# Optimization experiments

Hardware: AMD Instinct MI355X
Metric: run time of the kernel (lower is better)

## Reference

```python
import jax, jax.numpy as jnp
import numpy as np

L = 4
B_LIST = [30, 17, 9, 5, 3]      # bandwidth schedule (geometric 30 -> 3)
F_LIST = [1, 2, 5, 12, 28, 64]  # channel schedule (geometric 1 -> 64)
BATCH = 32
C64 = jnp.complex64

# near-identity grids (beta = pi/16, 6 alphas; SO3 grid additionally 6 gammas)
_A6 = np.linspace(0.0, 2 * np.pi, 6, endpoint=False)
S2_BETA = np.full(6, np.pi / 16)
S2_ALPHA = _A6
_aa, _gg = np.meshgrid(_A6, _A6, indexing='ij')
SO3_ALPHA = _aa.ravel()
SO3_BETA = np.full(36, np.pi / 16)
SO3_GAMMA = _gg.ravel()


def betas_of(b):
    return np.pi * (2 * np.arange(2 * b) + 1) / (4 * b)


def quad_weights(b):
    j = np.arange(2 * b)
    k = np.arange(b)
    s = (np.sin(np.pi * np.outer(2 * j + 1, 2 * k + 1) / (4 * b)) / (2 * k + 1)).sum(1)
    return (2.0 / b) * np.sin(np.pi * (2 * j + 1) / (4 * b)) * s


def wigner_d_all(lmax, betas):
    """Wigner small-d d^l_{m',m}(beta) via exp(-i beta Jy); list_l of [nbeta,2l+1,2l+1]."""
    out = [np.ones((len(betas), 1, 1))]
    for l in range(1, lmax):
        m = np.arange(-l, l)
        jp = np.sqrt(l * (l + 1) - m * (m + 1))  # <m+1|J+|m>
        Jy = np.zeros((2 * l + 1, 2 * l + 1), np.complex128)
        i = np.arange(2 * l)
        Jy[i + 1, i] = -0.5j * jp
        Jy[i, i + 1] = 0.5j * jp
        lam, U = np.linalg.eigh(Jy)
        ph = np.exp(-1j * np.outer(betas, lam))
        out.append(np.einsum('ak,bk,ck->bac', U, ph, U.conj()).real)
    return out


def fft_idx(l, n):
    # indices of frequencies m = -l..l in fft ordering of length n
    return np.concatenate([np.arange(n - l, n), np.arange(l + 1)])


def s2_fft(x, b_out):
    # x: [B,f,2b,2b] real (beta,alpha) -> list_l of [B,f,2l+1] complex
    b_in = x.shape[-1] // 2
    wig = wigner_d_all(b_out, betas_of(b_in))
    w = quad_weights(b_in)
    xf = jnp.fft.fft(x, axis=-1)
    out = []
    for l in range(b_out):
        dl = jnp.asarray((wig[l][:, :, l] * w[:, None]).astype(np.complex64))  # [2b,2l+1]
        out.append(jnp.einsum('bfjm,jm->bfm', xf[..., fft_idx(l, 2 * b_in)], dl))
    return out


def so3_fft(x, b_out):
    # x: [B,f,2b,2b,2b] real (beta,alpha,gamma) -> list_l of [B,f,2l+1,2l+1]
    b_in = x.shape[-1] // 2
    wig = wigner_d_all(b_out, betas_of(b_in))
    w = quad_weights(b_in)
    xf = jnp.fft.fft2(x, axes=(-2, -1))
    out = []
    for l in range(b_out):
        idx = fft_idx(l, 2 * b_in)
        dl = jnp.asarray((wig[l] * w[:, None, None]).astype(np.complex64))
        out.append(jnp.einsum('bfjmn,jmn->bfmn', xf[:, :, :, idx[:, None], idx[None, :]], dl))
    return out


def so3_ifft(coeffs, b):
    # coeffs: list_l [B,f,2l+1,2l+1] -> real signal [B,f,2b,2b,2b]
    wig = wigner_d_all(b, betas_of(b))
    nb = 2 * b
    Bz, f = coeffs[0].shape[:2]
    X = jnp.zeros((Bz, f, nb, nb, nb), C64)
    for l in range(b):
        idx = fft_idx(l, nb)
        dl = jnp.asarray(((2 * l + 1) * wig[l]).astype(np.complex64))
        X = X.at[:, :, :, idx[:, None], idx[None, :]].add(
            jnp.einsum('bfmn,jmn->bfjmn', coeffs[l], dl))
    return (jnp.fft.ifft2(X, axes=(-2, -1)) * (nb * nb)).real


def s2_kernel_ft(k, b):
    # k: [f_in,f_out,P] -> list_l of [2l+1,f_in,f_out] complex
    wig = wigner_d_all(b, S2_BETA)
    kc = k.astype(C64)
    out = []
    for l in range(b):
        m = np.arange(-l, l + 1)
        F = (wig[l][:, :, l] * np.exp(1j * np.outer(S2_ALPHA, m))).astype(np.complex64)
        out.append(jnp.einsum('iop,pm->mio', kc, jnp.asarray(F)))
    return out


def so3_kernel_ft(k, b):
    # k: [f_in,f_out,P] -> list_l of [2l+1,2l+1,f_in,f_out] complex
    wig = wigner_d_all(b, SO3_BETA)
    kc = k.astype(C64)
    out = []
    for l in range(b):
        m = np.arange(-l, l + 1)
        F = (wig[l]
             * np.exp(1j * np.outer(SO3_ALPHA, m))[:, :, None]
             * np.exp(1j * np.outer(SO3_GAMMA, m))[:, None, :]).astype(np.complex64)
        out.append(jnp.einsum('iop,pmn->mnio', kc, jnp.asarray(F)))
    return out


def s2_conv(x, kern, b_out):
    xh = s2_fft(x, b_out)
    kh = s2_kernel_ft(kern, b_out)
    yh = [jnp.einsum('bim,nio->bomn', xh[l], kh[l].conj()) for l in range(b_out)]
    return so3_ifft(yh, b_out)


def so3_conv(x, kern, b_out):
    xh = so3_fft(x, b_out)
    kh = so3_kernel_ft(kern, b_out)
    yh = [jnp.einsum('bimk,nkio->bomn', xh[l], kh[l].conj()) for l in range(b_out)]
    return so3_ifft(yh, b_out)


def so3_integrate(x):
    b = x.shape[-1] // 2
    w = jnp.asarray(quad_weights(b).astype(np.float32))
    return jnp.einsum('bfjac,j->bf', x, w) / float((2 * b) ** 2)


def batchnorm(x, g, be):
    mu = x.mean(0)
    var = ((x - mu) ** 2).mean(0)
    return (x - mu) * jax.lax.rsqrt(var + 1e-5) * g + be


def setup_inputs() -> dict:
    key = jax.random.key(0)
    ks = jax.random.split(key, 10)
    rn = lambda k, s, sc=1.0: jax.random.normal(k, s, jnp.float32) * sc
    return {
        'x': rn(ks[0], (BATCH, 1, 60, 60)),
        'k_s2': rn(ks[1], (1, 2, 6), 0.5),
        'k1': rn(ks[2], (2, 5, 36), 0.1),
        'k2': rn(ks[3], (5, 12, 36), 0.1),
        'k3': rn(ks[4], (12, 28, 36), 0.1),
        'k4': rn(ks[5], (28, 64, 36), 0.1),
        'g1': jnp.ones(64), 'be1': jnp.zeros(64),
        'w1': rn(ks[6], (64, 64), 0.125), 'b1': jnp.zeros(64),
        'g2': jnp.ones(64), 'be2': jnp.zeros(64),
        'w2': rn(ks[7], (64, 32), 0.125), 'b2': jnp.zeros(32),
        'g3': jnp.ones(32), 'be3': jnp.zeros(32),
        'w3': rn(ks[8], (32, 10), 0.18), 'b3': jnp.zeros(10),
    }


def reference(x, k_s2, k1, k2, k3, k4, g1, be1, w1, b1, g2, be2, w2, b2, g3, be3, w3, b3):
    h = jax.nn.relu(s2_conv(x, k_s2, B_LIST[0]))            # [B,2,60,60,60]
    for k, bo in zip((k1, k2, k3, k4), B_LIST[1:]):
        h = jax.nn.relu(so3_conv(h, k, bo))                 # bandwidth shrinks 17,9,5,3
    h = so3_integrate(h)                                    # [B,64]
    h = jax.nn.relu(batchnorm(h, g1, be1) @ w1 + b1)
    h = jax.nn.relu(batchnorm(h, g2, be2) @ w2 + b2)
    return batchnorm(h, g3, be3) @ w3 + b3                  # [B,10]
```

## Files before the change

kernel.cpp:

```cpp
#include <hip/hip_runtime.h>
#include <cmath>
#include <cstring>
#include <vector>


#define DPI 3.14159265358979323846

static constexpr int OQh(int l) { return l*(4*l*l - 1)/3; }
static_assert(OQh(30) == 35990, "oq30");
static_assert(OQh(17) == 6545,  "oq17");
static_assert(OQh(9)  == 969,   "oq9");
static_assert(OQh(5)  == 165,   "oq5");
static_assert(OQh(3)  == 35,    "oq3");

static constexpr int T1SUM = 18445;
static constexpr int T2SUM = 3417;

static constexpr size_t al256(size_t x){ return (x + 255) & ~(size_t)255; }
static constexpr size_t WS_XF1  = 0;
static constexpr size_t WS_XH1  = WS_XF1  + al256(32ull*60*30*8);
static constexpr size_t WS_KH1  = WS_XH1  + al256(32ull*900*8);
static constexpr size_t WS_XT2  = WS_KH1  + al256(1800ull*8);
static constexpr size_t WS_XH2  = WS_XT2  + al256(561ull*3840*8);
static constexpr size_t WS_KH2  = WS_XH2  + al256(64ull*6545*8);
// ... 273 lines not shown
  std::vector<double> tmp((size_t)59*59);

  { auto bs = betas(30);
    for (int l = 0; l < 30; l++) { int W = 2*l+1;
      for (int j = 0; j < 60; j++) {
        B.buildD(l, bs[j], tmp.data());
        for (int mm = -l; mm <= l; mm++)
          for (int nn = 0; nn <= l; nn++) {
            int am = mm < 0 ? -mm : mm;
            int lmin = am > nn ? am : nn;
            int term = HI[IO_TOFF1 + (mm+29)*30 + nn] + (l - lmin);
            HF[CO.dT1 + (size_t)term*60 + j] =
              (float)((2*l+1)*tmp[(size_t)(mm+l)*W + (nn+l)]);
          }
        if (l < 17) {
          for (int rem = 0; rem < W*W; rem++)
            HF[CO.dAT2 + (size_t)(OQh(l)+rem)*60 + j] = (float)(tmp[rem]*w30[j]);
        }
        float* dA1 = HF.data() + CO.A1 + 60ull*l*l + (size_t)j*W;
        for (int mi = 0; mi < W; mi++) dA1[mi] = (float)(tmp[(size_t)mi*W + l]*w30[j]);
      } } }
  { auto bs = betas(17);
    for (int l = 0; l < 17; l++) { int W = 2*l+1;
      for (int j = 0; j < 34; j++) {
        B.buildD(l, bs[j], tmp.data());
        for (int mm = -l; mm <= l; mm++)
          for (int nn = 0; nn <= l; nn++) {
            int am = mm < 0 ? -mm : mm;
            int lmin = am > nn ? am : nn;
            int term = HI[IO_TOFF2 + (mm+16)*17 + nn] + (l - lmin);
            HF[CO.dT2 + (size_t)term*34 + j] =
              (float)((2*l+1)*tmp[(size_t)(mm+l)*W + (nn+l)]);
          }
        if (l < 9) {
          for (int rem = 0; rem < W*W; rem++)
            HF[CO.dAT3 + (size_t)(OQh(l)+rem)*34 + j] = (float)(tmp[rem]*w17[j]);
        } } } }
  { auto bs = betas(9);
    for (int l = 0; l < 9; l++) { int W = 2*l+1;
      for (int j = 0; j < 18; j++) {
        B.buildD(l, bs[j], tmp.data());
        float* dst = HF.data() + CO.S3 + 18ull*OQh(l) + (size_t)j*W*W;
        for (int i2 = 0; i2 < W*W; i2++) dst[i2] = (float)((2*l+1)*tmp[i2]);
        if (l < 5) {
          float* dA = HF.data() + CO.A4 + 18ull*OQh(l) + (size_t)j*W*W;
          for (int i2 = 0; i2 < W*W; i2++) dA[i2] = (float)(tmp[i2]*w9[j]);
        } } } }
  { auto bs = betas(5);
    for (int l = 0; l < 5; l++) { int W = 2*l+1;
      for (int j = 0; j < 10; j++) {
        B.buildD(l, bs[j], tmp.data());
        float* dst = HF.data() + CO.S4 + 10ull*OQh(l) + (size_t)j*W*W;
        for (int i2 = 0; i2 < W*W; i2++) dst[i2] = (float)((2*l+1)*tmp[i2]);
        if (l < 3) {
          float* dA = HF.data() + CO.A5 + 10ull*OQh(l) + (size_t)j*W*W;
          for (int i2 = 0; i2 < W*W; i2++) dA[i2] = (float)(tmp[i2]*w5[j]);
        } } } }
  { auto bs = betas(3);
    for (int l = 0; l < 3; l++) { int W = 2*l+1;
      for (int j = 0; j < 6; j++) {
        B.buildD(l, bs[j], tmp.data());
        float* dst = HF.data() + CO.S5 + 6ull*OQh(l) + (size_t)j*W*W;
        for (int i2 = 0; i2 < W*W; i2++) dst[i2] = (float)((2*l+1)*tmp[i2]);
      } } }
  { double beta = DPI/16.0;
    for (int l = 0; l < 30; l++) { int n = 2*l+1;
      B.buildD(l, beta, tmp.data());
      for (int p = 0; p < 6; p++) {
        double al = 2.0*DPI*p/6.0;
        for (int mi = 0; mi < n; mi++) {
          double ph = al*(double)(mi - l);
          double dr = tmp[(size_t)mi*n + l];
          size_t off = CO.Fs2 + 6ull*l*l + (size_t)p*n + mi;
          HC[2*off]   = (float)(dr*cos(ph));
          HC[2*off+1] = (float)(dr*sin(ph));
        } }
      if (l < 17) {
        for (int p = 0; p < 36; p++) {
          double al = 2.0*DPI*(p/6)/6.0, ga = 2.0*DPI*(p%6)/6.0;
          for (int mi = 0; mi < n; mi++)
            for (int ni = 0; ni < n; ni++) {
              double ph = al*(double)(mi - l) + ga*(double)(ni - l);
              double dr = tmp[(size_t)mi*n + ni];
              size_t off = CO.Fso3 + 36ull*OQh(l) + (size_t)p*n*n + (size_t)mi*n + ni;
              HC[2*off]   = (float)(dr*cos(ph));
              HC[2*off+1] = (float)(dr*sin(ph));
            } } } } }
  auto fillTw = [&](size_t ofs, int N){
    for (int t = 0; t < N; t++) {
      HC[2*(ofs+t)]   = (float)cos(2.0*DPI*t/N);
      HC[2*(ofs+t)+1] = (float)sin(2.0*DPI*t/N);
    } };
  fillTw(CO.Tw60, 60); fillTw(CO.Tw34, 34);
  fillTw(CO.Tw18, 18); fillTw(CO.Tw10, 10); fillTw(CO.Tw6, 6);
  auto fillWn = [&](size_t ofs, int BQ, int N){
    for (int n = 0; n < BQ; n++)
      for (int cc2 = 0; cc2 < N; cc2++) {
        double f = (n == 0) ? 1.0 : 2.0;
        HC[2*(ofs + (size_t)n*N + cc2)]   = (float)(f*cos(2.0*DPI*n*cc2/N));
        HC[2*(ofs + (size_t)n*N + cc2)+1] = (float)(f*sin(2.0*DPI*n*cc2/N));
      } };
  auto fillWg = [&](size_t ofs, int N, int KT){
    for (int cc2 = 0; cc2 < N; cc2++)
      for (int k = 0; k < KT; k++) {
        HC[2*(ofs + (size_t)cc2*KT + k)]   = (float)cos(2.0*DPI*k*cc2/N);
        HC[2*(ofs + (size_t)cc2*KT + k)+1] = (float)(-sin(2.0*DPI*k*cc2/N));
      } };
  fillWn(CO.Wn1, 30, 60); fillWn(CO.Wn2o, 17, 34);
  fillWn(CO.Wn4, 5, 10);  fillWn(CO.Wn5, 3, 6);
  fillWg(CO.Wg1, 60, 17); fillWg(CO.Wg2, 34, 9); fillWg(CO.Wg4, 10, 3);
  for (int p = 0; p < 33; p++)
    for (int a = 0; a < 60; a++) {
      double th = 2.0*DPI*(p-16)*a/60.0;
      HC[2*(CO.WC1 + (size_t)p*60 + a)]   = (float)cos(th);
      HC[2*(CO.WC1 + (size_t)p*60 + a)+1] = (float)sin(th);
    }
  for (int p = 0; p < 17; p++)
    for (int a = 0; a < 34; a++) {
      double th = 2.0*DPI*(p-8)*a/34.0;
      HC[2*(CO.WC2 + (size_t)p*34 + a)]   = (float)cos(th);
      HC[2*(CO.WC2 + (size_t)p*34 + a)+1] = (float)sin(th);
    }
  for (int pm = 0; pm < 59; pm++)
    for (int a = 0; a < 30; a++) {
      int s = ((pm - 29) % 60 + 60) % 60;
      double th = 2.0*DPI*a*s/60.0;
      HC[2*(CO.WEO1 + (size_t)pm*30 + a)]   = (float)cos(th);
      HC[2*(CO.WEO1 + (size_t)pm*30 + a)+1] = (float)sin(th);
    }
  for (int pm = 0; pm < 33; pm++)
    for (int a = 0; a < 17; a++) {
      int s = ((pm - 16) % 34 + 34) % 34;
      double th = 2.0*DPI*a*s/34.0;
      HC[2*(CO.WEO2 + (size_t)pm*17 + a)]   = (float)cos(th);
      HC[2*(CO.WEO2 + (size_t)pm*17 + a)+1] = (float)sin(th);
    }
  for (int j = 0; j < 6; j++) HF[CO.WInt + j] = (float)(w3[j]/36.0);

  size_t fb  = CO.nF * sizeof(float);
  size_t fbA = al256(fb);
  size_t cb  = CO.nC * sizeof(float2);
  size_t cbA = al256(cb);
  size_t ib  = HI.size() * sizeof(int);
  void* base = nullptr;
  if (hipMalloc(&base, fbA + cbA + ib) != hipSuccess || !base) return;
  if (hipMemcpy(base, HF.data(), fb, hipMemcpyHostToDevice) != hipSuccess) return;
  if (hipMemcpy((char*)base + fbA, HC.data(), cb, hipMemcpyHostToDevice) != hipSuccess) return;
  if (hipMemcpy((char*)base + fbA + cbA, HI.data(), ib, hipMemcpyHostToDevice) != hipSuccess) return;
  (void)hipDeviceSynchronize();
  g_devF = (float*)base;
  g_devC = (float2*)((char*)base + fbA);
  g_devI = (int*)((char*)base + fbA + cbA);
}
namespace { struct InitOnce { InitOnce(){ build_all(); } } g_once; }

__device__ __forceinline__ int OQ(int l) { return l*(4*l*l - 1)/3; }
__device__ __forceinline__ int lFromQ(int q, int L) {
  int l = 0;
  while (l+1 < L && OQ(l+1) <= q) l++;
  return l;
}
__device__ __forceinline__ int lsq(int q) {
  int l = (int)sqrtf((float)q);
  while ((l+1)*(l+1) <= q) l++;
  while (l*l > q) l--;
  return l;
}
__device__ __forceinline__ void rotf(float2& r, float2 s) {
  float t = r.x*s.x - r.y*s.y;
  r.y = r.x*s.y + r.y*s.x;
  r.x = t;
}

__device__ __forceinline__ void kh_so3_one(int id, int L, int fi, int fo,
    const float* __restrict__ kk, const float2* __restrict__ F, float2* __restrict__ kh)
{
  int ff = fi*fo;
  int q = id / ff, r = id - q*ff;
  int i = r / fo, o = r - i*fo;
  int l = lFromQ(q, L); int W = 2*l+1; int W21 = W*W;
  int rem = q - OQ(l);
  const float2* Fb = F + 36ull*OQ(l) + rem;
  const float* kb = kk + (size_t)(i*fo + o)*36;
  float ax = 0.f, ay = 0.f;
  for (int p = 0; p < 36; p++) {
    float kv = kb[p];
    float2 f = Fb[(size_t)p*W21];
    ax += kv*f.x; ay += kv*f.y;
  }
  kh[(size_t)q*ff + r] = make_float2(ax, ay);
}

__global__ __launch_bounds__(256) void k_kh_all(
    const float* __restrict__ ks2, const float* __restrict__ k1,
    const float* __restrict__ k2,  const float* __restrict__ k3,
    const float* __restrict__ k4,
    const float2* __restrict__ Fs2, const float2* __restrict__ Fso3,
    float2* __restrict__ kh1, float2* __restrict__ kh2, float2* __restrict__ kh3,
    float2* __restrict__ kh4, float2* __restrict__ kh5)
{
  int id = blockIdx.x*256 + threadIdx.x;
  if (id < 1800) {
    int q = id >> 1, o = id & 1;
    int l = lsq(q); int W = 2*l+1; int mi = q - l*l;
    const float2* Fb = Fs2 + 6ull*l*l;
    float ax = 0.f, ay = 0.f;
    for (int p = 0; p < 6; p++) {
      float kv = ks2[o*6 + p];
      float2 f = Fb[p*W + mi];
      ax += kv*f.x; ay += kv*f.y;
    }
    kh1[(size_t)q*2 + o] = make_float2(ax, ay);
    return;
  }
  id -= 1800;
  if (id < OQh(17)*10) { kh_so3_one(id, 17, 2, 5, k1, Fso3, kh2); return; }
  id -= OQh(17)*10;
  if (id < OQh(9)*60) { kh_so3_one(id, 9, 5, 12, k2, Fso3, kh3); return; }
  id -= OQh(9)*60;
  if (id < OQh(5)*336) { kh_so3_one(id, 5, 12, 28, k3, Fso3, kh4); return; }
  id -= OQh(5)*336;
  if (id < OQh(3)*1792) { kh_so3_one(id, 3, 28, 64, k4, Fso3, kh5); return; }
}

__global__ __launch_bounds__(64) void k_s1_fftA(
    const float* __restrict__ x, const float2* __restrict__ tw, float2* __restrict__ XF1)
{
  __shared__ float row[60];
  int b = blockIdx.x / 60, j = blockIdx.x - b*60;
  int t = threadIdx.x;
  if (t < 60) row[t] = x[((size_t)b*60 + j)*60 + t];
  __syncthreads();
  if (t < 30) {
    float ax = 0.f, ay = 0.f;
    int ti = 0;
    for (int a = 0; a < 60; a++) {
      float2 w = tw[ti];
      ax += row[a]*w.x; ay -= row[a]*w.y;
      ti += t; if (ti >= 60) ti -= 60;
    }
    XF1[((size_t)b*60 + j)*30 + t] = make_float2(ax, ay);
  }
}

__global__ __launch_bounds__(256) void k_s1_coef(
    const float2* __restrict__ XF1, const float* __restrict__ dA1, float2* __restrict__ xh1)
{
  int id = blockIdx.x*blockDim.x + threadIdx.x;
  if (id >= 32*900) return;
  int b = id / 900, q = id - b*900;
  int l = lsq(q); int W = 2*l+1; int mi = q - l*l; int m = mi - l;
  const float* dp = dA1 + 60ull*l*l + mi;
  const float2* xb = XF1 + (size_t)b*60*30;
  int ma = m >= 0 ? m : -m;
  float sg = m >= 0 ? 1.f : -1.f;
  float ax = 0.f, ay = 0.f;
  for (int j = 0; j < 60; j++) {
    float2 xf = xb[j*30 + ma];
    float d = dp[(size_t)j*W];
    ax += d*xf.x; ay += sg*d*xf.y;
  }
  xh1[id] = make_float2(ax, ay);
}

__global__ __launch_bounds__(256) void k_yh_t(
    const float2* __restrict__ xh, const float2* __restrict__ kh,
    float2* __restrict__ yht, int L, int fi, int fo, int Qtot)
{
  int id = blockIdx.x*256 + threadIdx.x;
  int BOF = 32*fo;
  if (id >= Qtot*BOF) return;
  int q = id / BOF, bo = id - q*BOF;
  int b = bo / fo, o = bo - b*fo;
  int l = lFromQ(q, L); int W = 2*l+1;
  int rem = q - OQ(l); int mi = rem / W, ni = rem - mi*W;
  int ff = fi*fo;
  const float2* xb = xh + ((size_t)b*fi)*Qtot + OQ(l) + mi*W;
  const float2* kb = kh + ((size_t)(OQ(l) + ni*W))*ff + o;
  float ax = 0.f, ay = 0.f;
  for (int i = 0; i < fi; i++) {
    const float2* xrow = xb + (size_t)i*Qtot;
    const float2* krow = kb + (size_t)i*fo;
    for (int k = 0; k < W; k++) {
      float2 xv = xrow[k];
      float2 kv = krow[(size_t)k*ff];
      ax += xv.x*kv.x + xv.y*kv.y;
      ay += xv.y*kv.x - xv.x*kv.y;
    }
  }
  yht[id] = make_float2(ax, ay);
}

template<int BQ, int NJ, int BO, int CHSL, int STAGE1>
__global__ __launch_bounds__(256) void k_scatB(
    const float2* __restrict__ src,
    const float2* __restrict__ khp,
    const float* __restrict__ dT, const int* __restrict__ toff,
    const float2* __restrict__ WEO, float2* __restrict__ Tm, int slBase)
{
  constexpr int W2 = 2*BQ - 1;
  constexpr int TILES = CHSL/64;
  constexpr int PG = (BQ + 3)/4;
  __shared__ float2 P[W2*64];
  __shared__ float2 Wl[W2*BQ];
  __shared__ float2 kcl[STAGE1 ? 2*BQ : 2];
  const int tid = threadIdx.x;
  const int g = tid >> 6, lane = tid & 63;
  int n = blockIdx.x / TILES, ts = blockIdx.x - n*TILES;
  int slL = ts*64 + lane;
  int slG = slBase + slL;
  int bo = slG / NJ;
  int j  = slG - bo*NJ;

  for (int i = tid; i < W2*BQ; i += 256) Wl[i] = WEO[i];
  if constexpr (STAGE1) {
    int cnt = 2*(BQ - n);
    if (tid < cnt) {
      int l = n + (tid >> 1), o = tid & 1;
      kcl[2*l + o] = khp[(size_t)(l*l + n + l)*2 + o];
    }
  }
  __syncthreads();

  for (int pm = g; pm < W2; pm += 4) {
    int m = pm - (BQ-1);
    int am = m < 0 ? -m : m;
    int lmin = am > n ? am : n;
    int K = BQ - lmin;
    int tof = toff[pm*BQ + n];
    const float* dp = dT + (size_t)tof*NJ + j;
    float ax = 0.f, ay = 0.f;
    if constexpr (STAGE1) {
      int b = bo >> 1, o = bo & 1;
      const float2* xb = src + (size_t)b*900;
      for (int li = 0; li < K; li++) {
        int l = lmin + li;
        float d = dp[(size_t)li*NJ];
        float2 xv = xb[l*l + m + l];
        float2 kv = kcl[2*l + o];
        float yx = xv.x*kv.x + xv.y*kv.y;
        float yy = xv.y*kv.x - xv.x*kv.y;
        ax = fmaf(d, yx, ax); ay = fmaf(d, yy, ay);
      }
    } else {
      for (int li = 0; li < K; li++) {
        int l = lmin + li;
        int e = OQ(l) + (m+l)*(2*l+1) + (n+l);
        float d = dp[(size_t)li*NJ];
        float2 y = src[(size_t)e*BO + bo];
        ax = fmaf(d, y.x, ax); ay = fmaf(d, y.y, ay);
      }
    }
    P[pm*64 + lane] = make_float2(ax, ay);
  }
  __syncthreads();

  int a0 = g*PG;
  int cnt = BQ - a0; if (cnt > PG) cnt = PG; if (cnt < 0) cnt = 0;
  float2 E[PG], Od[PG];
  #pragma unroll
  for (int i = 0; i < PG; i++) { E[i] = make_float2(0.f,0.f); Od[i] = make_float2(0.f,0.f); }
  for (int t2 = 0; t2 < BQ; t2++) {
    float2 p = P[(2*t2)*64 + lane];
    const float2* wr = &Wl[(2*t2)*BQ + a0];
    #pragma unroll
    for (int i = 0; i < PG; i++) {
      float2 w = wr[i];
      E[i].x = fmaf(p.x, w.x, fmaf(-p.y, w.y, E[i].x));
      E[i].y = fmaf(p.x, w.y, fmaf( p.y, w.x, E[i].y));
    }
  }
  for (int t2 = 0; t2 < BQ-1; t2++) {
    float2 p = P[(2*t2+1)*64 + lane];
    const float2* wr = &Wl[(2*t2+1)*BQ + a0];
    #pragma unroll
    for (int i = 0; i < PG; i++) {
      float2 w = wr[i];
      Od[i].x = fmaf(p.x, w.x, fmaf(-p.y, w.y, Od[i].x));
      Od[i].y = fmaf(p.x, w.y, fmaf( p.y, w.x, Od[i].y));
    }
  }
  constexpr bool QS = ((BQ-1) & 1) != 0;
  for (int i = 0; i < cnt; i++) {
    int a = a0 + i;
    float2 tp = make_float2(E[i].x + Od[i].x, E[i].y + Od[i].y);
    float2 tq = QS ? make_float2(Od[i].x - E[i].x, Od[i].y - E[i].y)
                   : make_float2(E[i].x - Od[i].x, E[i].y - Od[i].y);
    Tm[((size_t)a*BQ + n)*CHSL + slL] = tp;
    Tm[((size_t)(a+BQ)*BQ + n)*CHSL + slL] = tq;
  }
}

template<int BQ, int KT, int CHSL>
__global__ __launch_bounds__(256) void k_dftB2(
    const float2* __restrict__ Tm, const float2* __restrict__ Wn,
    const float2* __restrict__ Wg, float2* __restrict__ U)
{
  constexpr int N = 2*BQ;
  constexpr int NH = BQ;
  constexpr int TILES = CHSL/64;
  __shared__ float2 WnL[BQ*NH];
  __shared__ float2 WgL[NH*KT];
  int a4 = blockIdx.x / TILES, ts = blockIdx.x - a4*TILES;
  int tid = threadIdx.x;
  int g = tid >> 6, lane = tid & 63;
  int a = a4*4 + g;
  for (int i = tid; i < BQ*NH; i += 256) { int nn = i/NH, c = i - nn*NH; WnL[i] = Wn[(size_t)nn*N + c]; }
  for (int i = tid; i < NH*KT; i += 256) WgL[i] = Wg[i];
  __syncthreads();
  if (a >= N) return;
  int sl = ts*64 + lane;
  float SE[NH], SO[NH];
  #pragma unroll
  for (int c = 0; c < NH; c++) { SE[c] = 0.f; SO[c] = 0.f; }
  const float2* Tb = Tm + (size_t)a*BQ*CHSL + sl;
  for (int t2 = 0; 2*t2 < BQ; t2++) {
    int nn = 2*t2;
    float2 tv = Tb[(size_t)nn*CHSL];
    #pragma unroll
    for (int c = 0; c < NH; c++) {
      float2 w = WnL[nn*NH + c];
      SE[c] = fmaf(tv.x, w.x, fmaf(-tv.y, w.y, SE[c]));
    }
  }
  for (int t2 = 0; 2*t2+1 < BQ; t2++) {
    int nn = 2*t2 + 1;
    float2 tv = Tb[(size_t)nn*CHSL];
    #pragma unroll
    for (int c = 0; c < NH; c++) {
      float2 w = WnL[nn*NH + c];
      SO[c] = fmaf(tv.x, w.x, fmaf(-tv.y, w.y, SO[c]));
    }
  }
  #pragma unroll
  for (int c = 0; c < NH; c++) {
    float s0 = fmaxf(SE[c] + SO[c], 0.f);
    float s1 = fmaxf(SE[c] - SO[c], 0.f);
    SE[c] = s0 + s1;
    SO[c] = s0 - s1;
  }
  float2* Ub = U + (size_t)a*KT*CHSL + sl;
  for (int k = 0; k < KT; k += 2) {
    float ux = 0.f, uy = 0.f;
    #pragma unroll
    for (int c = 0; c < NH; c++) {
      float2 w = WgL[c*KT + k];
      ux = fmaf(SE[c], w.x, ux); uy = fmaf(SE[c], w.y, uy);
    }
    Ub[(size_t)k*CHSL] = make_float2(ux, uy);
  }
  for (int k = 1; k < KT; k += 2) {
    float ux = 0.f, uy = 0.f;
    #pragma unroll
    for (int c = 0; c < NH; c++) {
      float2 w = WgL[c*KT + k];
      ux = fmaf(SO[c], w.x, ux); uy = fmaf(SO[c], w.y, uy);
    }
    Ub[(size_t)k*CHSL] = make_float2(ux, uy);
  }
}

template<int MT, int KT, int NH, int CHSL>
__global__ __launch_bounds__(256) void k_dftC2(
    const float2* __restrict__ U, const float2* __restrict__ WC,
    float2* __restrict__ xt, int slOff, int SLfull)
{
  constexpr int NA = 2*NH;
  constexpr int TILES = CHSL/64;
  constexpr int PGp = (MT + 3)/4;
  __shared__ float2 Us[NA*64];
  __shared__ float2 WcL[NH*MT];
  int k = blockIdx.x / TILES, ts = blockIdx.x - k*TILES;
  int tid = threadIdx.x;
  int g = tid >> 6, lane = tid & 63;
  for (int i = tid; i < NA*64; i += 256) {
    int aa = i >> 6, ll = i & 63;
    Us[i] = U[((size_t)aa*KT + k)*CHSL + ts*64 + ll];
  }
  for (int i = tid; i < NH*MT; i += 256) { int aa = i/MT, p = i - aa*MT; WcL[i] = WC[(size_t)p*NA + aa]; }
  __syncthreads();
  int p0 = g*PGp;
  int cnt = MT - p0; if (cnt > PGp) cnt = PGp; if (cnt < 0) cnt = 0;
  float2 acc[PGp];
  #pragma unroll
  for (int i = 0; i < PGp; i++) acc[i] = make_float2(0.f, 0.f);
  for (int aa = 0; aa < NH; aa++) {
    float2 u  = Us[aa*64 + lane];
    float2 u2 = Us[(aa+NH)*64 + lane];
    float2 vp = make_float2(u.x + u2.x, u.y + u2.y);
    float2 vm = make_float2(u.x - u2.x, u.y - u2.y);
    const float2* wr = &WcL[aa*MT + p0];
    #pragma unroll
    for (int i = 0; i < PGp; i++) {
      float2 w = wr[i];
      float2 v = ((p0 + i) & 1) ? vm : vp;
      acc[i].x = fmaf(v.x, w.x, fmaf( v.y, w.y, acc[i].x));
      acc[i].y = fmaf(v.y, w.x, fmaf(-v.x, w.y, acc[i].y));
    }
  }
  int sl = ts*64 + lane;
  for (int i = 0; i < cnt; i++) {
    int p = p0 + i;
    xt[((size_t)(p*KT + k))*SLfull + slOff + sl] = acc[i];
  }
}

template<int NBI, int NJ, int PAD, int QTOT>
__global__ __launch_bounds__(256) void k_coefg(
    const float2* __restrict__ xt, const float* __restrict__ dAT,
    const int* __restrict__ qoff, const int* __restrict__ qlist,
    float2* __restrict__ xh, int SLfull)
{
  __shared__ float re[NBI*PAD], im[NBI*PAD];
  int pr = blockIdx.x;
  const float2* row = xt + (size_t)pr*SLfull;
  for (int idx = threadIdx.x; idx < NBI*NJ; idx += 256) {
    int bi = idx / NJ, j = idx - bi*NJ;
    float2 v = row[idx];
    re[bi*PAD + j] = v.x; im[bi*PAD + j] = v.y;
  }
  __syncthreads();
  int o0 = qoff[pr], nq = qoff[pr+1] - o0;
  int w = threadIdx.x >> 6, lane = threadIdx.x & 63;
  for (int i = w; i < nq; i += 4) {
    int e = qlist[o0 + i];
    int q = e >> 1;
    float sg = (e & 1) ? -1.f : 1.f;
    const float* dp = dAT + (size_t)q*NJ;
    for (int bi = lane; bi < NBI; bi += 64) {
      float ax = 0.f, ay = 0.f;
      const float* rr = &re[bi*PAD];
      const float* ii = &im[bi*PAD];
      #pragma unroll 4
      for (int j = 0; j < NJ; j++) {
        float d = dp[j];
        ax = fmaf(d, rr[j], ax);
        ay = fmaf(d, ii[j], ay);
      }
      xh[(size_t)bi*QTOT + q] = make_float2(ax, sg*ay);
    }
  }
}

__global__ __launch_bounds__(256) void k_coef(
    const float2* __restrict__ xt, const float* __restrict__ dA,
    float2* __restrict__ xh, int L, int nj, int KT, int MT, int Qtot, int nbi)
{
  int id = blockIdx.x*blockDim.x + threadIdx.x;
  if (id >= nbi*Qtot) return;
  int bi = id / Qtot, q = id - bi*Qtot;
  int l = lFromQ(q, L); int W = 2*l+1; int W21 = W*W;
  int rem = q - OQ(l); int mi = rem / W, ki = rem - mi*W;
  int m = mi - l, ks = ki - l;
  const float* dAp = dA + (size_t)nj*OQ(l) + rem;
  int MTKT = MT*KT;
  int pidx; float sgn;
  if (ks >= 0) { pidx = (m + (KT-1))*KT + ks;  sgn =  1.f; }
  else         { pidx = (-m + (KT-1))*KT - ks; sgn = -1.f; }
  const float2* xb = xt + (size_t)bi*nj*MTKT + pidx;
  float ax = 0.f, ay = 0.f;
  for (int j = 0; j < nj; j++) {
    float2 xv = xb[(size_t)j*MTKT];
    float d = dAp[(size_t)j*W21];
    ax += d*xv.x; ay += sgn*d*xv.y;
  }
  xh[id] = make_float2(ax, ay);
}

template<int BQ, int N, int KT, int MT, int TPB, int BO>
__global__ __launch_bounds__(TPB) void k_synth3(
    const float2* __restrict__ yh, const float* __restrict__ dS,
    const float2* __restrict__ twN, float2* __restrict__ xt)
{
  constexpr int W2  = 2*BQ - 1;
  constexpr int NH  = N/2;
  constexpr int CP  = (BQ+3) & ~3;
  constexpr int KTP = (KT+1) & ~1;
  constexpr int R3  = (N%4 == 0) ? 4 : 2;
  constexpr int RP  = (NH%2 == 0) ? 2 : 1;
  constexpr int SZA0 = (W2*CP*8 > 2*N*NH*4) ? W2*CP*8 : 2*N*NH*4;
  constexpr int SZA  = (SZA0 + 15) & ~15;
  constexpr int SZB0 = (N*CP*8 > 2*NH*KTP*8) ? N*CP*8 : 2*NH*KTP*8;
  constexpr int SZB  = (SZB0 + 15) & ~15;
  __shared__ __align__(16) char smem[SZA + SZB + N*8];
  float2* P   = (float2*)smem;
  float*  SS  = (float*)smem;
  float*  SD  = SS + N*NH;
  float2* Tm  = (float2*)(smem + SZA);
  float2* USS = (float2*)(smem + SZA);
  float2* USD = USS + NH*KTP;
  float2* twl = (float2*)(smem + SZA + SZB);

  const int tid = threadIdx.x;
  int nwg = gridDim.x, bidx = blockIdx.x;
  int per = nwg >> 3;
  int swz = (bidx & 7)*per + (bidx >> 3);
  int bo = swz / N, j = swz - bo*N;

  for (int t = tid; t < N; t += TPB) twl[t] = twN[t];

  for (int idx = tid; idx < W2*CP; idx += TPB) {
    int pm = idx / CP, n = idx - pm*CP;
    float ax = 0.f, ay = 0.f;
    if (n < BQ) {
      int m = pm - (BQ-1);
      int am = m < 0 ? -m : m;
      int lmin = am > n ? am : n;
      int base = lmin*(4*lmin*lmin - 1)/3;
      for (int l = lmin; l < BQ; l++) {
        int Wl = 2*l+1;
        int e = base + (m+l)*Wl + (n+l);
        float2 y = yh[(size_t)e*BO + bo];
        float d = dS[(size_t)N*base + (size_t)j*Wl*Wl + (m+l)*Wl + (n+l)];
        ax += d*y.x; ay += d*y.y;
        base += Wl*Wl;
      }
    }
    P[idx] = make_float2(ax, ay);
  }
  __syncthreads();

  {
    constexpr int CG = CP/4;
    constexpr float SGN = ((BQ-1) & 1) ? -1.f : 1.f;
    const float4* P4 = (const float4*)P;
    for (int it = tid; it < NH*CG; it += TPB) {
      int a = it / CG, cg = it - a*CG;
      float2 s2 = twl[2*a];
      float2 r = make_float2(1.f, 0.f);
      float4 E0 = {0,0,0,0}, E1 = {0,0,0,0}, O0 = {0,0,0,0}, O1 = {0,0,0,0};
      for (int jj = 0; jj < BQ-1; jj++) {
        float4 e0 = P4[(2*jj)*(CP/2) + 2*cg];
        float4 e1 = P4[(2*jj)*(CP/2) + 2*cg + 1];
        float4 o0 = P4[(2*jj+1)*(CP/2) + 2*cg];
        float4 o1 = P4[(2*jj+1)*(CP/2) + 2*cg + 1];
        E0.x += e0.x*r.x - e0.y*r.y; E0.y += e0.x*r.y + e0.y*r.x;
        E0.z += e0.z*r.x - e0.w*r.y; E0.w += e0.z*r.y + e0.w*r.x;
        E1.x += e1.x*r.x - e1.y*r.y; E1.y += e1.x*r.y + e1.y*r.x;
        E1.z += e1.z*r.x - e1.w*r.y; E1.w += e1.z*r.y + e1.w*r.x;
        O0.x += o0.x*r.x - o0.y*r.y; O0.y += o0.x*r.y + o0.y*r.x;
        O0.z += o0.z*r.x - o0.w*r.y; O0.w += o0.z*r.y + o0.w*r.x;
        O1.x += o1.x*r.x - o1.y*r.y; O1.y += o1.x*r.y + o1.y*r.x;
        O1.z += o1.z*r.x - o1.w*r.y; O1.w += o1.z*r.y + o1.w*r.x;
        rotf(r, s2);
      }
      {
        float4 e0 = P4[(2*(BQ-1))*(CP/2) + 2*cg];
        float4 e1 = P4[(2*(BQ-1))*(CP/2) + 2*cg + 1];
        E0.x += e0.x*r.x - e0.y*r.y; E0.y += e0.x*r.y + e0.y*r.x;
        E0.z += e0.z*r.x - e0.w*r.y; E0.w += e0.z*r.y + e0.w*r.x;
        E1.x += e1.x*r.x - e1.y*r.y; E1.y += e1.x*r.y + e1.y*r.x;
        E1.z += e1.z*r.x - e1.w*r.y; E1.w += e1.z*r.y + e1.w*r.x;
      }
      float2 wa = twl[a];
      int pidx = (N - (a*(BQ-1)) % N) % N;
      float2 ph = twl[pidx];
      int c0 = 4*cg;
      auto doCol = [&](float ex, float ey, float ox, float oy, int col) {
        float gx = ox*wa.x - oy*wa.y, gy = ox*wa.y + oy*wa.x;
        float px = ex + gx, py = ey + gy;
        float qx = ex - gx, qy = ey - gy;
        Tm[a*CP + col]        = make_float2(px*ph.x - py*ph.y, px*ph.y + py*ph.x);
        Tm[(a+NH)*CP + col]   = make_float2(SGN*(qx*ph.x - qy*ph.y), SGN*(qx*ph.y + qy*ph.x));
      };
      doCol(E0.x, E0.y, O0.x, O0.y, c0+0);
      doCol(E0.z, E0.w, O0.z, O0.w, c0+1);
      doCol(E1.x, E1.y, O1.x, O1.y, c0+2);
      doCol(E1.z, E1.w, O1.z, O1.w, c0+3);
    }
  }
  __syncthreads();

  {
    constexpr int NO3 = BQ/2;
    constexpr int NRG = N/R3;
    for (int it = tid; it < NRG*NH; it += TPB) {
      int rg = it / NH, c = it - rg*NH;
// ... 411 lines not shown
```

Before: 825.6 us.

## Swizzle scatter blocks across XCDs, unroll l-loop, read twiddles from global

In k_scatB the block index is remapped so consecutive tiles of the same n land on the same XCD, which should improve L2 reuse of the shared d-table and source data on the multi-XCD MI355X. The inner l-reduction loops are manually unrolled by four so several independent global loads can be in flight at once. The shared-memory copy of the WEO twiddle matrix is dropped and the values are read straight from global memory (uniform, cached reads). This saves LDS and a sync-bound preload, but adds global-load latency inside the FMA loop.

```diff
diff --git a/kernel.cpp b/kernel.cpp
--- a/kernel.cpp
+++ b/kernel.cpp
@@ -599,17 +599,21 @@
   constexpr int TILES = CHSL/64;
   constexpr int PG = (BQ + 3)/4;
   __shared__ float2 P[W2*64];
-  __shared__ float2 Wl[W2*BQ];
   __shared__ float2 kcl[STAGE1 ? 2*BQ : 2];
   const int tid = threadIdx.x;
   const int g = tid >> 6, lane = tid & 63;
-  int n = blockIdx.x / TILES, ts = blockIdx.x - n*TILES;
+
+  int nwg = gridDim.x;
+  int q8 = nwg >> 3, r8 = nwg & 7;
+  int xcd = blockIdx.x & 7, off = blockIdx.x >> 3;
+  int swz = (xcd < r8 ? xcd*(q8+1) : r8*(q8+1) + (xcd-r8)*q8) + off;
+  int n = swz / TILES, ts = swz - n*TILES;
+
   int slL = ts*64 + lane;
   int slG = slBase + slL;
   int bo = slG / NJ;
   int j  = slG - bo*NJ;
 
-  for (int i = tid; i < W2*BQ; i += 256) Wl[i] = WEO[i];
   if constexpr (STAGE1) {
     int cnt = 2*(BQ - n);
     if (tid < cnt) {
@@ -624,23 +628,59 @@
     int am = m < 0 ? -m : m;
     int lmin = am > n ? am : n;
     int K = BQ - lmin;
-    int tof = toff[pm*BQ + n];
-    const float* dp = dT + (size_t)tof*NJ + j;
+    const float* dp = dT + (size_t)toff[pm*BQ + n]*NJ + j;
     float ax = 0.f, ay = 0.f;
     if constexpr (STAGE1) {
       int b = bo >> 1, o = bo & 1;
       const float2* xb = src + (size_t)b*900;
-      for (int li = 0; li < K; li++) {
+      int li = 0;
+      for (; li + 4 <= K; li += 4) {
+        int l0 = lmin + li;
+        float d0 = dp[(size_t)(li+0)*NJ];
+        float d1 = dp[(size_t)(li+1)*NJ];
+        float d2 = dp[(size_t)(li+2)*NJ];
+        float d3 = dp[(size_t)(li+3)*NJ];
+        float2 x0 = xb[l0*(l0+1) + m];
+        float2 x1 = xb[(l0+1)*(l0+2) + m];
+        float2 x2 = xb[(l0+2)*(l0+3) + m];
+        float2 x3 = xb[(l0+3)*(l0+4) + m];
+        float2 c0 = kcl[2*l0 + o], c1 = kcl[2*(l0+1) + o];
+        float2 c2 = kcl[2*(l0+2) + o], c3 = kcl[2*(l0+3) + o];
+        ax = fmaf(d0, x0.x*c0.x + x0.y*c0.y, ax); ay = fmaf(d0, x0.y*c0.x - x0.x*c0.y, ay);
+        ax = fmaf(d1, x1.x*c1.x + x1.y*c1.y, ax); ay = fmaf(d1, x1.y*c1.x - x1.x*c1.y, ay);
+        ax = fmaf(d2, x2.x*c2.x + x2.y*c2.y, ax); ay = fmaf(d2, x2.y*c2.x - x2.x*c2.y, ay);
+        ax = fmaf(d3, x3.x*c3.x + x3.y*c3.y, ax); ay = fmaf(d3, x3.y*c3.x - x3.x*c3.y, ay);
+      }
+      for (; li < K; li++) {
         int l = lmin + li;
         float d = dp[(size_t)li*NJ];
-        float2 xv = xb[l*l + m + l];
+        float2 xv = xb[l*(l+1) + m];
         float2 kv = kcl[2*l + o];
-        float yx = xv.x*kv.x + xv.y*kv.y;
-        float yy = xv.y*kv.x - xv.x*kv.y;
-        ax = fmaf(d, yx, ax); ay = fmaf(d, yy, ay);
+        ax = fmaf(d, xv.x*kv.x + xv.y*kv.y, ax);
+        ay = fmaf(d, xv.y*kv.x - xv.x*kv.y, ay);
       }
     } else {
-      for (int li = 0; li < K; li++) {
+      int li = 0;
+      for (; li + 4 <= K; li += 4) {
+        int l0 = lmin + li;
+        int e0 = OQ(l0)     + (m+l0)*(2*l0+1)   + (n+l0);
+        int e1 = OQ(l0+1)   + (m+l0+1)*(2*l0+3) + (n+l0+1);
+        int e2 = OQ(l0+2)   + (m+l0+2)*(2*l0+5) + (n+l0+2);
+        int e3 = OQ(l0+3)   + (m+l0+3)*(2*l0+7) + (n+l0+3);
+        float d0 = dp[(size_t)(li+0)*NJ];
+        float d1 = dp[(size_t)(li+1)*NJ];
+        float d2 = dp[(size_t)(li+2)*NJ];
+        float d3 = dp[(size_t)(li+3)*NJ];
+        float2 y0 = src[(size_t)e0*BO + bo];
+        float2 y1 = src[(size_t)e1*BO + bo];
+        float2 y2 = src[(size_t)e2*BO + bo];
+        float2 y3 = src[(size_t)e3*BO + bo];
+        ax = fmaf(d0, y0.x, ax); ay = fmaf(d0, y0.y, ay);
+        ax = fmaf(d1, y1.x, ax); ay = fmaf(d1, y1.y, ay);
+        ax = fmaf(d2, y2.x, ax); ay = fmaf(d2, y2.y, ay);
+        ax = fmaf(d3, y3.x, ax); ay = fmaf(d3, y3.y, ay);
+      }
+      for (; li < K; li++) {
         int l = lmin + li;
         int e = OQ(l) + (m+l)*(2*l+1) + (n+l);
         float d = dp[(size_t)li*NJ];
@@ -659,7 +699,7 @@
   for (int i = 0; i < PG; i++) { E[i] = make_float2(0.f,0.f); Od[i] = make_float2(0.f,0.f); }
   for (int t2 = 0; t2 < BQ; t2++) {
     float2 p = P[(2*t2)*64 + lane];
-    const float2* wr = &Wl[(2*t2)*BQ + a0];
+    const float2* wr = &WEO[(size_t)(2*t2)*BQ + a0];
     #pragma unroll
     for (int i = 0; i < PG; i++) {
       float2 w = wr[i];
@@ -669,7 +709,7 @@
   }
   for (int t2 = 0; t2 < BQ-1; t2++) {
     float2 p = P[(2*t2+1)*64 + lane];
-    const float2* wr = &Wl[(2*t2+1)*BQ + a0];
+    const float2* wr = &WEO[(size_t)(2*t2+1)*BQ + a0];
     #pragma unroll
     for (int i = 0; i < PG; i++) {
       float2 w = wr[i];
```

Result: slower. 904.7 us (+9.6%).
